# Kernel tuning notes

Hardware: AMD Instinct MI355X
Metric: run time of the kernel (lower is better)

The kernel has to match this reference:

```python
import jax, jax.numpy as jnp
import numpy as np
from jax import lax

NUM_C = 100
EMB = 256
B = 64
L = 500
NSTU = 4096
N = NUM_C + 1  # skill_embedding rows / GCN node count


def gcn_conv(x, src, dst, W, b):
    # PyG GCNConv: add self-loops, symmetric deg^-1/2 norm, scatter-add at target.
    # x: [N, Fin]; src, dst: [E] (duplicates kept, as in PyG); W: [Fout, Fin]
    n = x.shape[0]
    loop = jnp.arange(n)
    s = jnp.concatenate([src, loop])
    d = jnp.concatenate([dst, loop])
    deg = jnp.zeros((n,), x.dtype).at[d].add(1.0)
    dinv = jnp.where(deg > 0, lax.rsqrt(deg), 0.0)
    norm = dinv[s] * dinv[d]  # [E+N]
    h = x @ W.T
    out = jnp.zeros((n, h.shape[1]), x.dtype).at[d].add(norm[:, None] * h[s])
    return out + b


def rnn(x, Wih, Whh, bih, bhh):
    # torch.nn.RNN (tanh, batch_first): h_t = tanh(x_t Wih^T + bih + h_{t-1} Whh^T + bhh)
    h0 = jnp.zeros((x.shape[0], Whh.shape[0]), x.dtype)
    def step(h, xt):
        h = jnp.tanh(xt @ Wih.T + bih + h @ Whh.T + bhh)
        return h, h
    _, hs = lax.scan(step, h0, jnp.swapaxes(x, 0, 1))
    return jnp.swapaxes(hs, 0, 1)


def next_pred(res, skill):
    # (res * one_hot(next_skill)).sum(-1); row NUM_C of the one-hot table is all-zero padding
    ns = skill[:, 1:]
    p = jnp.take_along_axis(res, jnp.minimum(ns, NUM_C - 1)[..., None], axis=-1)[..., 0]
    return jnp.where(ns == NUM_C, 0.0, p)


def _forward(student, skill, answer, G, skill_emb, answer_emb, stu,
             hg_w1, hg_b1, hg_w2, hg_b2, gcn_w1, gcn_b1, gcn_w2, gcn_b2,
             w1_w, w1_b, w2_w, w2_b, fc_d_w, fc_d_b, fc_h_w, fc_h_b,
             fc_e_w, fc_e_b, pos, dg_wih, dg_whh, dg_bih, dg_bhh,
             hgr_wih, hgr_whh, hgr_bih, hgr_bhh):
    mask = (answer != 2)[..., None].astype(jnp.float32)  # [B,L,1]
    src, dst = skill[:, :-1], skill[:, 1:]               # per-sample edge lists [B,L-1]

    # HGNN over student hypergraph (eval mode: dropout = identity): x' = G (x W + b)
    h = jax.nn.relu(G @ (stu @ hg_w1.T + hg_b1))
    stu_embedding = G @ (h @ hg_w2.T + hg_b2)            # [NSTU, EMB]

    se = skill_emb[skill]                                # [B,L,EMB]
    ae = answer_emb[answer]
    skill_answer = jnp.concatenate([se, ae], -1)
    answer_skill = jnp.concatenate([ae, se], -1)
    stu_h = stu_embedding[student - 1]                   # one_hot @ table == gather, [B,L,EMB]

    # per-sample 2-layer GCN over the shared skill embedding table, vmapped over batch
    gcn2 = jax.vmap(lambda s, d: gcn_conv(
        jax.nn.relu(gcn_conv(skill_emb, s, d, gcn_w1, gcn_b1)), s, d, gcn_w2, gcn_b2))
    all_h = gcn2(src, dst)                               # [B,N,EMB]

    g = jnp.take_along_axis(all_h, skill[..., None], axis=1) * mask  # [B,L,EMB]
    lengths = mask.sum(axis=1)[:, 0].astype(jnp.int32)   # effective lengths [B]
    expand_pos = pos[lengths - 1]                        # [B,L,1] (L==500)
    expand_pos = jax.nn.softmax(expand_pos * mask, axis=1)
    pooled = (g * expand_pos).sum(axis=1)                # [B,EMB]
    pooled = jnp.broadcast_to(pooled[:, None, :], (B, L, EMB))

    x = jnp.where((answer == 1)[..., None], skill_answer, answer_skill)  # [B,L,2E]
    h_dg = rnn(jnp.concatenate([pooled, x], -1), dg_wih, dg_whh, dg_bih, dg_bhh)
    h_hg = rnn(jnp.concatenate([stu_h, x], -1), hgr_wih, hgr_whh, hgr_bih, hgr_bhh)

    logit_h = h_hg @ fc_h_w.T + fc_h_b
    logit_d = h_dg @ fc_d_w.T + fc_d_b
    theta = jax.nn.sigmoid(h_hg @ w1_w.T + w1_b + h_dg @ w2_w.T + w2_b)
    ens = jnp.concatenate([theta * h_hg, (1.0 - theta) * h_dg], -1) @ fc_e_w.T + fc_e_b
    return (next_pred(logit_h[:, :-1], skill),
            next_pred(logit_d[:, :-1], skill),
            next_pred(ens[:, :-1], skill))


def setup_inputs() -> dict:
    key = jax.random.key(0)
    ks = jax.random.split(key, 24)
    f = lambda i, shape, s=0.05: jax.random.normal(ks[i], shape, jnp.float32) * s
    return {
        "student": jax.random.randint(ks[0], (B, L), 1, NSTU + 1),
        "skill": jax.random.randint(ks[1], (B, L), 0, N),
        "answer": jax.random.randint(ks[2], (B, L), 0, 3),
        "G": f(3, (NSTU, NSTU), 0.01),
        "skill_emb": f(4, (N, EMB), 1.0),
        "answer_emb": f(5, (3, EMB), 1.0),
        "stu": f(6, (NSTU, EMB), 1.0),
        "hg_w1": f(7, (EMB, EMB)), "hg_b1": jnp.zeros((EMB,), jnp.float32),
        "hg_w2": f(8, (EMB, EMB)), "hg_b2": jnp.zeros((EMB,), jnp.float32),
        "gcn_w1": f(9, (8, EMB)), "gcn_b1": jnp.zeros((8,), jnp.float32),
        "gcn_w2": f(10, (EMB, 8)), "gcn_b2": jnp.zeros((EMB,), jnp.float32),
        "w1_w": f(11, (EMB, EMB)), "w1_b": jnp.zeros((EMB,), jnp.float32),
        "w2_w": f(12, (EMB, EMB)), "w2_b": jnp.zeros((EMB,), jnp.float32),
        "fc_d_w": f(13, (NUM_C, EMB)), "fc_d_b": jnp.zeros((NUM_C,), jnp.float32),
        "fc_h_w": f(14, (NUM_C, EMB)), "fc_h_b": jnp.zeros((NUM_C,), jnp.float32),
        "fc_e_w": f(15, (NUM_C, 2 * EMB)), "fc_e_b": jnp.zeros((NUM_C,), jnp.float32),
        "pos": jax.random.uniform(ks[16], (500, 500, 1), jnp.float32),
        "dg_wih": f(17, (EMB, 3 * EMB)), "dg_whh": f(18, (EMB, EMB)),
        "dg_bih": jnp.zeros((EMB,), jnp.float32), "dg_bhh": jnp.zeros((EMB,), jnp.float32),
        "hgr_wih": f(19, (EMB, 3 * EMB)), "hgr_whh": f(20, (EMB, EMB)),
        "hgr_bih": jnp.zeros((EMB,), jnp.float32), "hgr_bhh": jnp.zeros((EMB,), jnp.float32),
    }


def reference(student, skill, answer, G, skill_emb, answer_emb, stu,
              hg_w1, hg_b1, hg_w2, hg_b2, gcn_w1, gcn_b1, gcn_w2, gcn_b2,
              w1_w, w1_b, w2_w, w2_b, fc_d_w, fc_d_b, fc_h_w, fc_h_b,
              fc_e_w, fc_e_b, pos, dg_wih, dg_whh, dg_bih, dg_bhh,
              hgr_wih, hgr_whh, hgr_bih, hgr_bhh):
    return _forward(student, skill, answer, G, skill_emb, answer_emb, stu,
                    hg_w1, hg_b1, hg_w2, hg_b2, gcn_w1, gcn_b1, gcn_w2, gcn_b2,
                    w1_w, w1_b, w2_w, w2_b, fc_d_w, fc_d_b, fc_h_w, fc_h_b,
                    fc_e_w, fc_e_b, pos, dg_wih, dg_whh, dg_bih, dg_bhh,
                    hgr_wih, hgr_whh, hgr_bih, hgr_bhh)
```

## Files before the change

kernel.cpp:

```cpp
#include <hip/hip_runtime.h>
#include <cstdint>
#include <cstddef>

typedef unsigned short u16;
typedef __attribute__((ext_vector_type(8))) short short8;
typedef __attribute__((ext_vector_type(4))) short short4v;
typedef __attribute__((ext_vector_type(4))) float f32x4;

__device__ __forceinline__ float b2f(u16 u){ return __uint_as_float(((unsigned)u)<<16); }
__device__ __forceinline__ u16 f2b(float f){
    unsigned u = __float_as_uint(f);
    return (u16)((u + 0x7fffu + ((u>>16)&1u)) >> 16);
}
__device__ __forceinline__ int iclamp(int v, int lo, int hi){ return v<lo?lo:(v>hi?hi:v); }

__device__ __forceinline__ void barrier_lds(){
    asm volatile("s_waitcnt lgkmcnt(0)\n\ts_barrier" ::: "memory");
}

__device__ __forceinline__ float fast_exp2(float x){
#if __has_builtin(__builtin_amdgcn_exp2f)
    return __builtin_amdgcn_exp2f(x);
#else
    return __expf(x * 0.6931471805599453f);
#endif
}

__device__ __forceinline__ short8 ld8f(const float* p){
    f32x4 a = *(const f32x4*)p;
    f32x4 b = *(const f32x4*)(p+4);
    short8 r;
    #pragma unroll
    for(int j=0;j<4;j++){ r[j]=(short)f2b(a[j]); r[4+j]=(short)f2b(b[j]); }
    return r;
}
__device__ __forceinline__ short8 ld8f_s(const float* p, float s){
    f32x4 a = *(const f32x4*)p;
    f32x4 b = *(const f32x4*)(p+4);
    short8 r;
    #pragma unroll
    for(int j=0;j<4;j++){ r[j]=(short)f2b(a[j]*s); r[4+j]=(short)f2b(b[j]*s); }
    return r;
}
__device__ __forceinline__ short8 ld8b(const u16* p){ return *(const short8*)p; }

#define C_TANH 2.8853900817779268f

__global__ __launch_bounds__(256) void k_cvt(const float* __restrict__ in, u16* __restrict__ outp){
    const size_t i = ((size_t)blockIdx.x*256 + threadIdx.x)*8;
    *(short8*)&outp[i] = ld8f(in + i);
}

template<bool TRANSOUT, bool RELU, bool AF32, bool BF32>
__global__ __launch_bounds__(256) void gemm64(
    const void* __restrict__ A, const void* __restrict__ B,
    const float* __restrict__ bias, u16* __restrict__ C,
    int M, int N, int K, int ldb, int ldc)
{
    constexpr int BK=32;
    __shared__ u16 As[2][64][BK+8];
    __shared__ u16 Bs[2][64][BK+8];
    const int tid = threadIdx.x;
    const int bm = blockIdx.x*64, bn = blockIdx.y*64;
    const int wave = tid>>6, lane = tid&63, lm = lane&15, lg = lane>>4;
    const int wm = (wave>>1)*32, wn = (wave&1)*32;
    f32x4 acc[2][2];
    #pragma unroll
    for(int i=0;i<2;i++){ acc[i][0]=(f32x4){0.f,0.f,0.f,0.f}; acc[i][1]=(f32x4){0.f,0.f,0.f,0.f}; }

    const int arow = tid>>2, akc = (tid&3)*8;
    auto lda8 = [&](int k)->short8{
        return AF32 ? ld8f((const float*)A + (size_t)(bm+arow)*K + k+akc)
                    : ld8b((const u16*)A + (size_t)(bm+arow)*K + k+akc);
    };
    auto ldb8v = [&](int k)->short8{
        return BF32 ? ld8f((const float*)B + (size_t)(bn+arow)*ldb + k+akc)
                    : ld8b((const u16*)B + (size_t)(bn+arow)*ldb + k+akc);
    };
    *(short8*)&As[0][arow][akc] = lda8(0);
    *(short8*)&Bs[0][arow][akc] = ldb8v(0);
    barrier_lds();
    int p = 0;
    for(int k0=0;k0<K;k0+=BK){
        short8 a_n, b_n;
        const bool more = (k0+BK < K);
        if(more){ a_n = lda8(k0+BK); b_n = ldb8v(k0+BK); }
        short8 af[2], bfg[2];
        #pragma unroll
        for(int mt=0;mt<2;mt++) af[mt]  = *(const short8*)&As[p][wm+mt*16+lm][lg*8];
        #pragma unroll
        for(int nt=0;nt<2;nt++) bfg[nt] = *(const short8*)&Bs[p][wn+nt*16+lm][lg*8];
        #pragma unroll
        for(int nt=0;nt<2;nt++)
            #pragma unroll
            for(int mt=0;mt<2;mt++)
                acc[mt][nt] = __builtin_amdgcn_mfma_f32_16x16x32_bf16(af[mt], bfg[nt], acc[mt][nt], 0,0,0);
        if(more){
            *(short8*)&As[p^1][arow][akc] = a_n;
            *(short8*)&Bs[p^1][arow][akc] = b_n;
        }
        barrier_lds();
        p ^= 1;
    }
    #pragma unroll
    for(int nt=0;nt<2;nt++){
        const int col = bn+wn+nt*16+lm;
        const float bv = bias ? bias[col] : 0.f;
        #pragma unroll
        for(int mt=0;mt<2;mt++){
            const int row0 = bm+wm+mt*16+lg*4;
            #pragma unroll
            for(int r=0;r<4;r++){
                const int row = row0+r;
                float v = acc[mt][nt][r] + bv;
                if(RELU) v = fmaxf(v, 0.f);
                const size_t idx = TRANSOUT ? ((size_t)col*ldc + row) : ((size_t)row*ldc + col);
                C[idx] = f2b(v);
            }
        }
    }
}

__global__ __launch_bounds__(256) void k_h1pre(const float* __restrict__ skill_emb,
                                               const float* __restrict__ gcn_w1,
                                               float* __restrict__ h1pre)
{
    const int i = blockIdx.x*101 + threadIdx.x;
    if(threadIdx.x >= 101) return;
    const int idx = i; if(idx>=808) return;
    const int n=idx>>3, j=idx&7;
    const float* x = skill_emb + n*256;
    const float* w = gcn_w1 + j*256;
    float acc=0.f;
    for(int k=0;k<256;k+=4){
        f32x4 a = *(const f32x4*)&x[k];
        f32x4 b = *(const f32x4*)&w[k];
        acc += a.x*b.x + a.y*b.y + a.z*b.z + a.w*b.w;
    }
    h1pre[idx]=acc;
}

__global__ __launch_bounds__(256) void k_idx(const int* __restrict__ skill,
                                             const int* __restrict__ answer,
                                             const int* __restrict__ student,
                                             int* __restrict__ combo_t, int* __restrict__ sid_t)
{
    const int i = blockIdx.x*256 + threadIdx.x;
    if(i>=32000) return;
    const int t = i>>6, b = i&63;
    const int sk = iclamp(skill[b*500+t], 0, 100);
    const int an = iclamp(answer[b*500+t], 0, 2);
    const int sd = iclamp(student[b*500+t]-1, 0, 4095);
    combo_t[i] = sk*3+an;
    sid_t[i]   = sd;
}

__global__ __launch_bounds__(256) void k_gcn(
    const int* __restrict__ skill, const int* __restrict__ answer,
    const float* __restrict__ pos, const float* __restrict__ h1pre,
    const float* __restrict__ gcn_b1, const float* __restrict__ gcn_w2, const float* __restrict__ gcn_b2,
    float* __restrict__ pooled)
{
    const int b = blockIdx.x, tid = threadIdx.x;
    __shared__ int   sk[500];
    __shared__ float msk[500];
    __shared__ float coef[500];
    __shared__ float deg[101];
    __shared__ float agg1[101*8];
    __shared__ float agg2[101*8];
    __shared__ float red[256];
    __shared__ float vec8[8];
    __shared__ float sS[1];

    for(int i=tid;i<500;i+=256){
        sk[i]=iclamp(skill[b*500+i],0,100);
        msk[i] = (answer[b*500+i]!=2)?1.f:0.f;
    }
    for(int i=tid;i<101;i+=256) deg[i]=1.f;
    if(tid<8)  vec8[tid]=0.f;
    if(tid==8) sS[0]=0.f;
    __syncthreads();
    for(int e=tid;e<499;e+=256) atomicAdd(&deg[sk[e+1]], 1.f);
    __syncthreads();
    for(int i=tid;i<101;i+=256) deg[i] = rsqrtf(deg[i]);
    float cnt=0.f; for(int i=tid;i<500;i+=256) cnt += msk[i];
    __syncthreads();
    red[tid]=cnt; __syncthreads();
    for(int s=128;s>0;s>>=1){ if(tid<s) red[tid]+=red[tid+s]; __syncthreads(); }
    const int len = iclamp((int)(red[0]+0.5f), 1, 500);
    __syncthreads();
    for(int i=tid;i<808;i+=256){ const int n=i>>3; agg1[i] = deg[n]*deg[n]*h1pre[i]; }
    __syncthreads();
    for(int i=tid;i<499*8;i+=256){
        const int e=i>>3, j=i&7, s=sk[e], d=sk[e+1];
        atomicAdd(&agg1[d*8+j], deg[s]*deg[d]*h1pre[s*8+j]);
    }
    __syncthreads();
    for(int i=tid;i<808;i+=256){ const int j=i&7; agg1[i] = fmaxf(agg1[i]+gcn_b1[j], 0.f); }
    __syncthreads();
    for(int i=tid;i<808;i+=256){ const int n=i>>3; agg2[i] = deg[n]*deg[n]*agg1[i]; }
    __syncthreads();
    for(int i=tid;i<499*8;i+=256){
        const int e=i>>3, j=i&7, s=sk[e], d=sk[e+1];
        atomicAdd(&agg2[d*8+j], deg[s]*deg[d]*agg1[s*8+j]);
    }
    const size_t prow = (size_t)(len-1)*500;
    float vmax = -1e30f;
    for(int i=tid;i<500;i+=256){ const float v = pos[prow+i]*msk[i]; coef[i]=v; vmax=fmaxf(vmax,v); }
    red[tid]=vmax; __syncthreads();
    for(int s=128;s>0;s>>=1){ if(tid<s) red[tid]=fmaxf(red[tid],red[tid+s]); __syncthreads(); }
    const float m = red[0]; __syncthreads();
    float lsum=0.f;
    for(int i=tid;i<500;i+=256){ const float e=__expf(coef[i]-m); coef[i]=e; lsum+=e; }
    red[tid]=lsum; __syncthreads();
    for(int s=128;s>0;s>>=1){ if(tid<s) red[tid]+=red[tid+s]; __syncthreads(); }
    const float inv = 1.f/red[0];
    __syncthreads();
    float v8[8]={0,0,0,0,0,0,0,0}; float ls=0.f;
    for(int i=tid;i<500;i+=256){
        const float ci = coef[i]*inv*msk[i];
        if(ci!=0.f){
            const int n=sk[i]; ls+=ci;
            #pragma unroll
            for(int j=0;j<8;j++) v8[j] += ci*agg2[n*8+j];
        }
    }
    #pragma unroll
    for(int j=0;j<8;j++) atomicAdd(&vec8[j], v8[j]);
    atomicAdd(&sS[0], ls);
    __syncthreads();
    {
        const int o = tid;
        float acc = gcn_b2[o]*sS[0];
        #pragma unroll
        for(int j=0;j<8;j++) acc += vec8[j]*gcn_w2[o*8+j];
        pooled[b*256+o] = acc;
    }
}

__global__ __launch_bounds__(256) void k_table2(
    const float* __restrict__ skill_emb, const float* __restrict__ answer_emb,
    const float* __restrict__ wih_dg, const float* __restrict__ bih_dg, const float* __restrict__ bhh_dg,
    const float* __restrict__ wih_hg, const float* __restrict__ bih_hg, const float* __restrict__ bhh_hg,
    float* __restrict__ table_dg, float* __restrict__ table_hg)
{
    const int combo = blockIdx.x, tid = threadIdx.x, which = blockIdx.y;
    const float* wih = which ? wih_hg : wih_dg;
    const float* bih = which ? bih_hg : bih_dg;
    const float* bhh = which ? bhh_hg : bhh_dg;
    float* table     = which ? table_hg : table_dg;
    const int sid = combo/3, ans = combo - sid*3;
    __shared__ float sf[256], sg[256];
    sf[tid] = (ans==1) ? skill_emb[(size_t)sid*256+tid] : answer_emb[(size_t)ans*256+tid];
    sg[tid] = (ans==1) ? answer_emb[(size_t)ans*256+tid] : skill_emb[(size_t)sid*256+tid];
    __syncthreads();
    const int o = tid;
    float acc = bih[o] + bhh[o];
    const float* w = wih + (size_t)o*768;
    for(int k=0;k<256;k+=4){
        f32x4 w1v = *(const f32x4*)&w[256+k];
        f32x4 w2v = *(const f32x4*)&w[512+k];
        acc += sf[k]*w1v.x + sf[k+1]*w1v.y + sf[k+2]*w1v.z + sf[k+3]*w1v.w;
        acc += sg[k]*w2v.x + sg[k+1]*w2v.y + sg[k+2]*w2v.z + sg[k+3]*w2v.w;
    }
    table[(size_t)combo*256 + o] = acc;
}

__global__ __launch_bounds__(256) void k_pooledproj(const float* __restrict__ pooled,
                                                    const float* __restrict__ wih,
                                                    u16* __restrict__ outp)
{
    const int b=blockIdx.x, tid=threadIdx.x;
    __shared__ float p[256];
    p[tid] = pooled[b*256+tid];
    __syncthreads();
    const float* w = wih + (size_t)tid*768;
    float acc=0.f;
    for(int k=0;k<256;k+=4){
        f32x4 wv = *(const f32x4*)&w[k];
        acc += p[k]*wv.x + p[k+1]*wv.y + p[k+2]*wv.z + p[k+3]*wv.w;
    }
    outp[b*256+tid]=f2b(acc);
}

__global__ __launch_bounds__(256) void k_pre(
    const int* __restrict__ combo_t, const int* __restrict__ sid_t,
    const float* __restrict__ table_dg, const float* __restrict__ table_hg,
    const u16* __restrict__ pooled_proj, const u16* __restrict__ stu_proj,
    u16* __restrict__ pre_dg, u16* __restrict__ pre_hg)
{
    const int t = blockIdx.x, rnn = blockIdx.y, c = threadIdx.x;
    const int b0 = blockIdx.z*16;
    const float* tab = rnn ? table_hg : table_dg;
    u16* outp = rnn ? pre_hg : pre_dg;
    for(int b=b0;b<b0+16;b++){
        const int cmb = combo_t[t*64+b];
        const u16* prow = rnn ? (stu_proj + (size_t)sid_t[t*64+b]*256)
                              : (pooled_proj + (size_t)b*256);
        const float v = (tab[(size_t)cmb*256 + c] + b2f(prow[c])) * C_TANH;
        outp[((size_t)t*64+b)*256 + c] = f2b(v);
    }
}

__global__ __launch_bounds__(1024) void k_rnn(
    const u16* __restrict__ pre_dg, const u16* __restrict__ pre_hg,
    const float* __restrict__ whh_dg, const float* __restrict__ whh_hg,
    u16* __restrict__ hall_dg, u16* __restrict__ hall_hg)
{
    __shared__ u16 hc[2][8][4][16][8];
    const int bid = blockIdx.x;
    const int rnn = bid>>2, grp = bid&3, rb = grp*16;
    const float* W   = rnn ? whh_hg : whh_dg;
    const u16*  pre  = rnn ? pre_hg : pre_dg;
    u16*        out  = rnn ? hall_hg : hall_dg;
    const int tid = threadIdx.x, wave = tid>>6, lane = tid&63;
    const int lm = lane&15, lg = lane>>4;
    const int cb = wave*16;

    short8 wf[8];
    #pragma unroll
    for(int kk=0;kk<8;kk++)
        wf[kk] = ld8f_s(W + (size_t)(cb+lm)*256 + kk*32 + lg*8, C_TANH);

    for(int i=tid;i<2*8*4*16*8/2;i+=1024) ((unsigned*)hc)[i]=0;

    const size_t base = (size_t)(rb+lm)*256 + cb + lg*4;
    const int wchunk = wave>>1, wsub = (wave&1)*2 + (lg>>1), wslot = (lg&1)*4;

    const u16* pp = pre + base;
    u16*       op = out + base;
    uint2 pv = *(const uint2*)pp;
    pp += 16384;
    __syncthreads();

    auto stepf = [&](const u16 (&S)[8][4][16][8], u16 (&D)[8][4][16][8],
                     uint2 pvi, const u16* ppi, u16* opi)->uint2 {
        f32x4 a0, c0 = (f32x4){0.f,0.f,0.f,0.f};
        a0[0] = __uint_as_float(pvi.x << 16);
        a0[1] = __uint_as_float(pvi.x & 0xffff0000u);
        a0[2] = __uint_as_float(pvi.y << 16);
        a0[3] = __uint_as_float(pvi.y & 0xffff0000u);
        #pragma unroll
        for(int kk=0;kk<4;kk++){
            short8 hb = *(const short8*)&S[kk][lg][lm][0];
            a0 = __builtin_amdgcn_mfma_f32_16x16x32_bf16(wf[kk], hb, a0, 0,0,0);
        }
        #pragma unroll
        for(int kk=4;kk<8;kk++){
            short8 hb = *(const short8*)&S[kk][lg][lm][0];
            c0 = __builtin_amdgcn_mfma_f32_16x16x32_bf16(wf[kk], hb, c0, 0,0,0);
        }
        const uint2 pvn = *(const uint2*)ppi;
        float th[4];
        #pragma unroll
        for(int r=0;r<4;r++){
            const float x = a0[r] + c0[r];
            const float e = fast_exp2(x);
            th[r] = fmaf(-2.f, __builtin_amdgcn_rcpf(e + 1.f), 1.f);
        }
        uint2 pk;
        asm("v_cvt_pk_bf16_f32 %0, %1, %2" : "=v"(pk.x) : "v"(th[0]), "v"(th[1]));
        asm("v_cvt_pk_bf16_f32 %0, %1, %2" : "=v"(pk.y) : "v"(th[2]), "v"(th[3]));
        *(uint2*)&D[wchunk][wsub][lm][wslot] = pk;
        *(uint2*)opi = pk;
        barrier_lds();
        return pvn;
    };

    for(int t=0;t<500;t+=2){
        pv = stepf(hc[0], hc[1], pv, pp, op);  pp += 16384; op += 16384;
        pv = stepf(hc[1], hc[0], pv, pp, op);  pp += 16384; op += 16384;
    }
}

__global__ __launch_bounds__(256) void k_theta(
    const u16* __restrict__ Ah, const u16* __restrict__ Ad,
    const float* __restrict__ w1, const float* __restrict__ w2,
    const float* __restrict__ b1, const float* __restrict__ b2,
    u16* __restrict__ theta)
{
    constexpr int BK=32;
    __shared__ u16 AsH[128][BK+8];
    __shared__ u16 AsD[128][BK+8];
    __shared__ u16 BsH[64][BK+8];
    __shared__ u16 BsD[64][BK+8];
    const int tid = threadIdx.x;
    const int bm = blockIdx.x*128, bn = blockIdx.y*64;
    const int wave = tid>>6, lane = tid&63, lm = lane&15, lg = lane>>4;
    const int wm = (wave>>1)*64, wn = (wave&1)*32;
    f32x4 acc[4][2];
    #pragma unroll
    for(int i=0;i<4;i++){ acc[i][0]=(f32x4){0.f,0.f,0.f,0.f}; acc[i][1]=(f32x4){0.f,0.f,0.f,0.f}; }

    const int arow0 = tid>>2, akc0 = (tid&3)*8;
    const int arow1 = arow0 + 64;
    for(int k0=0;k0<256;k0+=BK){
        *(short8*)&AsH[arow0][akc0] = ld8b(Ah + (size_t)(bm+arow0)*256 + k0+akc0);
        *(short8*)&AsH[arow1][akc0] = ld8b(Ah + (size_t)(bm+arow1)*256 + k0+akc0);
        *(short8*)&AsD[arow0][akc0] = ld8b(Ad + (size_t)(bm+arow0)*256 + k0+akc0);
        *(short8*)&AsD[arow1][akc0] = ld8b(Ad + (size_t)(bm+arow1)*256 + k0+akc0);
        *(short8*)&BsH[arow0][akc0] = ld8f(w1 + (size_t)(bn+arow0)*256 + k0+akc0);
        *(short8*)&BsD[arow0][akc0] = ld8f(w2 + (size_t)(bn+arow0)*256 + k0+akc0);
        __syncthreads();
        short8 afH[4], afD[4], bf1[2], bf2[2];
        #pragma unroll
        for(int mt=0;mt<4;mt++){
            afH[mt] = *(const short8*)&AsH[wm+mt*16+lm][lg*8];
            afD[mt] = *(const short8*)&AsD[wm+mt*16+lm][lg*8];
        }
        #pragma unroll
        for(int nt=0;nt<2;nt++){
            bf1[nt] = *(const short8*)&BsH[wn+nt*16+lm][lg*8];
            bf2[nt] = *(const short8*)&BsD[wn+nt*16+lm][lg*8];
        }
        #pragma unroll
        for(int nt=0;nt<2;nt++)
            #pragma unroll
            for(int mt=0;mt<4;mt++){
                acc[mt][nt] = __builtin_amdgcn_mfma_f32_16x16x32_bf16(afH[mt], bf1[nt], acc[mt][nt], 0,0,0);
                acc[mt][nt] = __builtin_amdgcn_mfma_f32_16x16x32_bf16(afD[mt], bf2[nt], acc[mt][nt], 0,0,0);
            }
        __syncthreads();
    }
    #pragma unroll
    for(int nt=0;nt<2;nt++){
        const int col = bn+wn+nt*16+lm;
        const float bb = b1[col]+b2[col];
        #pragma unroll
        for(int mt=0;mt<4;mt++){
            const int row0 = bm+wm+mt*16+lg*4;
            #pragma unroll
            for(int r=0;r<4;r++){
                const float x = acc[mt][nt][r] + bb;
                theta[(size_t)(row0+r)*256 + col] = f2b(1.f/(1.f+__expf(-x)));
            }
        }
    }
}

__global__ __launch_bounds__(256) void k_out(
    const int* __restrict__ skill,
    const u16* __restrict__ hall_hg, const u16* __restrict__ hall_dg,
    const u16* __restrict__ theta,
    const float* __restrict__ fc_h_w, const float* __restrict__ fc_h_b,
    const float* __restrict__ fc_d_w, const float* __restrict__ fc_d_b,
    const float* __restrict__ fc_e_w, const float* __restrict__ fc_e_b,
    float* __restrict__ outp)
{
    const int tid=threadIdx.x, lane=tid&63;
    const int wid = blockIdx.x*4 + (tid>>6);
    const int b = wid/499, t = wid - b*499;
    const int ns = skill[b*500 + t + 1];
    float o0=0.f,o1=0.f,o2=0.f,bh=0.f,bd=0.f,be=0.f;
    if(ns != 100){
        const int c = iclamp(ns, 0, 99);
        const size_t r = (size_t)t*64 + b;
        const int k = lane*4;
        short4v hh  = *(const short4v*)&hall_hg[r*256+k];
        short4v hd  = *(const short4v*)&hall_dg[r*256+k];
        short4v th  = *(const short4v*)&theta[r*256+k];
        f32x4 fh  = *(const f32x4*)&fc_h_w[(size_t)c*256+k];
        f32x4 fd  = *(const f32x4*)&fc_d_w[(size_t)c*256+k];
        f32x4 fe1 = *(const f32x4*)&fc_e_w[(size_t)c*512+k];
        f32x4 fe2 = *(const f32x4*)&fc_e_w[(size_t)c*512+256+k];
        #pragma unroll
        for(int j=0;j<4;j++){
            const float hhj=b2f((u16)hh[j]), hdj=b2f((u16)hd[j]), tj=b2f((u16)th[j]);
            o0 += hhj*fh[j];
            o1 += hdj*fd[j];
            o2 += tj*hhj*fe1[j] + (1.f-tj)*hdj*fe2[j];
        }
        #pragma unroll
        for(int off=32;off>0;off>>=1){
            o0 += __shfl_down(o0,off);
            o1 += __shfl_down(o1,off);
            o2 += __shfl_down(o2,off);
        }
        bh=fc_h_b[c]; bd=fc_d_b[c]; be=fc_e_b[c];
    }
    if(lane==0){
        outp[            b*499+t] = (ns==100)?0.f:(o0+bh);
        outp[31936     + b*499+t] = (ns==100)?0.f:(o1+bd);
        outp[2*31936   + b*499+t] = (ns==100)?0.f:(o2+be);
    }
}

extern "C" void kernel_launch(void* const* d_in, const int* in_sizes, int n_in,
                              void* d_out, int out_size, void* d_ws, size_t ws_size,
                              hipStream_t stream)
{
    const int* student = (const int*)d_in[0];
    const int* skill   = (const int*)d_in[1];
    const int* answer  = (const int*)d_in[2];
    const float* G        = (const float*)d_in[3];
    const float* skill_emb= (const float*)d_in[4];
    const float* answer_emb=(const float*)d_in[5];
    const float* stu      = (const float*)d_in[6];
    const float* hg_w1    = (const float*)d_in[7];
    const float* hg_b1    = (const float*)d_in[8];
    const float* hg_w2    = (const float*)d_in[9];
    const float* hg_b2    = (const float*)d_in[10];
    const float* gcn_w1   = (const float*)d_in[11];
    const float* gcn_b1   = (const float*)d_in[12];
    const float* gcn_w2   = (const float*)d_in[13];
    const float* gcn_b2   = (const float*)d_in[14];
    const float* w1_w     = (const float*)d_in[15];
    const float* w1_b     = (const float*)d_in[16];
    const float* w2_w     = (const float*)d_in[17];
    const float* w2_b     = (const float*)d_in[18];
    const float* fc_d_w   = (const float*)d_in[19];
    const float* fc_d_b   = (const float*)d_in[20];
    const float* fc_h_w   = (const float*)d_in[21];
    const float* fc_h_b   = (const float*)d_in[22];
    const float* fc_e_w   = (const float*)d_in[23];
    const float* fc_e_b   = (const float*)d_in[24];
    const float* pos      = (const float*)d_in[25];
    const float* dg_wih   = (const float*)d_in[26];
    const float* dg_whh   = (const float*)d_in[27];
    const float* dg_bih   = (const float*)d_in[28];
    const float* dg_bhh   = (const float*)d_in[29];
    const float* hgr_wih  = (const float*)d_in[30];
    const float* hgr_whh  = (const float*)d_in[31];
    const float* hgr_bih  = (const float*)d_in[32];
    const float* hgr_bhh  = (const float*)d_in[33];

    char* ws = (char*)d_ws;
    size_t off = 0;
    auto nxt = [&](size_t bytes)->char*{
        char* r = ws + off;
        off += (bytes + 255) & ~(size_t)255;
        return r;
    };
    float* h1pre      = (float*)nxt(808*4);
    float* pooled     = (float*)nxt(64*256*4);
    float* table_dg   = (float*)nxt(303*256*4);
    float* table_hg   = (float*)nxt(303*256*4);
    u16*   tmpT       = (u16*)  nxt((size_t)256*4096*2);
    u16*   hbuf       = (u16*)  nxt((size_t)4096*256*2);
    u16*   stu_proj   = (u16*)  nxt((size_t)4096*256*2);
    u16*   pooled_proj= (u16*)  nxt(64*256*2);
    int*   combo_t    = (int*)  nxt(32000*4);
    int*   sid_t      = (int*)  nxt(32000*4);
    u16*   Gb         = (u16*)  nxt((size_t)4096*4096*2);
    u16*   hall_dg    = (u16*)  nxt((size_t)32000*256*2);
    u16*   hall_hg    = (u16*)  nxt((size_t)32000*256*2);
    u16*   pre_dg     = Gb;
    u16*   pre_hg     = Gb + (size_t)32000*256;
    u16*   theta      = pre_dg;

    k_h1pre<<<8,256,0,stream>>>(skill_emb, gcn_w1, h1pre);
    k_gcn<<<64,256,0,stream>>>(skill, answer, pos, h1pre, gcn_b1, gcn_w2, gcn_b2, pooled);
    k_table2<<<dim3(303,2),256,0,stream>>>(skill_emb, answer_emb,
                                           dg_wih, dg_bih, dg_bhh,
                                           hgr_wih, hgr_bih, hgr_bhh,
                                           table_dg, table_hg);
    k_idx<<<125,256,0,stream>>>(skill, answer, student, combo_t, sid_t);
    k_cvt<<<8192,256,0,stream>>>(G, Gb);

    gemm64<true ,false,true ,true ><<<dim3(64,4),256,0,stream>>>(stu,  hg_w1, hg_b1, tmpT, 4096,256,256,  256, 4096);
    gemm64<false,true ,false,false><<<dim3(64,4),256,0,stream>>>(Gb,   tmpT,  nullptr, hbuf, 4096,256,4096, 4096, 256);
    gemm64<true ,false,false,true ><<<dim3(64,4),256,0,stream>>>(hbuf, hg_w2, hg_b2, tmpT, 4096,256,256,  256, 4096);
    gemm64<false,false,false,false><<<dim3(64,4),256,0,stream>>>(Gb,   tmpT,  nullptr, hbuf, 4096,256,4096, 4096, 256);
    gemm64<false,false,false,true ><<<dim3(64,4),256,0,stream>>>(hbuf, hgr_wih, nullptr, stu_proj, 4096,256,256, 768, 256);

    k_pooledproj<<<64,256,0,stream>>>(pooled, dg_wih, pooled_proj);

    k_pre<<<dim3(500,2,4),256,0,stream>>>(combo_t, sid_t, table_dg, table_hg,
                                          pooled_proj, stu_proj, pre_dg, pre_hg);

    k_rnn<<<8,1024,0,stream>>>(pre_dg, pre_hg, dg_whh, hgr_whh, hall_dg, hall_hg);

    k_theta<<<dim3(250,4),256,0,stream>>>(hall_hg, hall_dg, w1_w, w2_w, w1_b, w2_b, theta);
    k_out<<<7984,256,0,stream>>>(skill, hall_hg, hall_dg, theta,
                                 fc_h_w, fc_h_b, fc_d_w, fc_d_b, fc_e_w, fc_e_b,
                                 (float*)d_out);
}
```

Baseline: 804.5 us.

## Fuse prep kernels, fold pooled projection into GCN, read fp32 G directly

Merges the table, index and h1pre kernels into one launch and folds the pooled-projection matvec into the GCN kernel's epilogue. It also drops the separate fp32-to-bf16 conversion of the 4096x4096 G matrix, so the two big GEMMs load fp32 G and convert it while staging tiles. This removes several launches and a 64MB read plus 32MB write conversion pass. The trade-off is that both G GEMMs now each read 64MB of fp32 instead of 32MB of bf16 and convert in the inner loop.

Measured after the change: 862.4 us. 1.07x slower.

```diff
diff --git a/kernel.cpp b/kernel.cpp
--- a/kernel.cpp
+++ b/kernel.cpp
@@ -45,11 +45,6 @@
 __device__ __forceinline__ short8 ld8b(const u16* p){ return *(const short8*)p; }
 
 #define C_TANH 2.8853900817779268f
-
-__global__ __launch_bounds__(256) void k_cvt(const float* __restrict__ in, u16* __restrict__ outp){
-    const size_t i = ((size_t)blockIdx.x*256 + threadIdx.x)*8;
-    *(short8*)&outp[i] = ld8f(in + i);
-}
 
 template<bool TRANSOUT, bool RELU, bool AF32, bool BF32>
 __global__ __launch_bounds__(256) void gemm64(
@@ -121,45 +116,70 @@
     }
 }
 
-__global__ __launch_bounds__(256) void k_h1pre(const float* __restrict__ skill_emb,
-                                               const float* __restrict__ gcn_w1,
-                                               float* __restrict__ h1pre)
-{
-    const int i = blockIdx.x*101 + threadIdx.x;
-    if(threadIdx.x >= 101) return;
-    const int idx = i; if(idx>=808) return;
-    const int n=idx>>3, j=idx&7;
-    const float* x = skill_emb + n*256;
-    const float* w = gcn_w1 + j*256;
-    float acc=0.f;
-    for(int k=0;k<256;k+=4){
-        f32x4 a = *(const f32x4*)&x[k];
-        f32x4 b = *(const f32x4*)&w[k];
-        acc += a.x*b.x + a.y*b.y + a.z*b.z + a.w*b.w;
-    }
-    h1pre[idx]=acc;
-}
-
-__global__ __launch_bounds__(256) void k_idx(const int* __restrict__ skill,
-                                             const int* __restrict__ answer,
-                                             const int* __restrict__ student,
-                                             int* __restrict__ combo_t, int* __restrict__ sid_t)
-{
-    const int i = blockIdx.x*256 + threadIdx.x;
-    if(i>=32000) return;
-    const int t = i>>6, b = i&63;
-    const int sk = iclamp(skill[b*500+t], 0, 100);
-    const int an = iclamp(answer[b*500+t], 0, 2);
-    const int sd = iclamp(student[b*500+t]-1, 0, 4095);
-    combo_t[i] = sk*3+an;
-    sid_t[i]   = sd;
+__global__ __launch_bounds__(256) void k_prep(
+    const float* __restrict__ skill_emb, const float* __restrict__ answer_emb,
+    const float* __restrict__ wih_dg, const float* __restrict__ bih_dg, const float* __restrict__ bhh_dg,
+    const float* __restrict__ wih_hg, const float* __restrict__ bih_hg, const float* __restrict__ bhh_hg,
+    const float* __restrict__ gcn_w1,
+    const int* __restrict__ skill, const int* __restrict__ answer, const int* __restrict__ student,
+    float* __restrict__ table_dg, float* __restrict__ table_hg,
+    float* __restrict__ h1pre, int* __restrict__ combo_t, int* __restrict__ sid_t)
+{
+    const int bid = blockIdx.x, tid = threadIdx.x;
+    if(bid < 606){
+        const int which = (bid >= 303) ? 1 : 0;
+        const int combo = bid - which*303;
+        const float* wih = which ? wih_hg : wih_dg;
+        const float* bih = which ? bih_hg : bih_dg;
+        const float* bhh = which ? bhh_hg : bhh_dg;
+        float* table     = which ? table_hg : table_dg;
+        const int sid = combo/3, ans = combo - sid*3;
+        __shared__ float sf[256], sg[256];
+        sf[tid] = (ans==1) ? skill_emb[(size_t)sid*256+tid] : answer_emb[(size_t)ans*256+tid];
+        sg[tid] = (ans==1) ? answer_emb[(size_t)ans*256+tid] : skill_emb[(size_t)sid*256+tid];
+        __syncthreads();
+        const int o = tid;
+        float acc = bih[o] + bhh[o];
+        const float* w = wih + (size_t)o*768;
+        for(int k=0;k<256;k+=4){
+            f32x4 w1v = *(const f32x4*)&w[256+k];
+            f32x4 w2v = *(const f32x4*)&w[512+k];
+            acc += sf[k]*w1v.x + sf[k+1]*w1v.y + sf[k+2]*w1v.z + sf[k+3]*w1v.w;
+            acc += sg[k]*w2v.x + sg[k+1]*w2v.y + sg[k+2]*w2v.z + sg[k+3]*w2v.w;
+        }
+        table[(size_t)combo*256 + o] = acc;
+    } else if(bid < 731){
+        const int i = (bid-606)*256 + tid;
+        if(i>=32000) return;
+        const int t = i>>6, b = i&63;
+        const int sk = iclamp(skill[b*500+t], 0, 100);
+        const int an = iclamp(answer[b*500+t], 0, 2);
+        const int sd = iclamp(student[b*500+t]-1, 0, 4095);
+        combo_t[i] = sk*3+an;
+        sid_t[i]   = sd;
+    } else {
+        if(tid >= 101) return;
+        const int idx = (bid-731)*101 + tid;
+        if(idx>=808) return;
+        const int n=idx>>3, j=idx&7;
+        const float* x = skill_emb + n*256;
+        const float* w = gcn_w1 + j*256;
+        float acc=0.f;
+        for(int k=0;k<256;k+=4){
+            f32x4 a = *(const f32x4*)&x[k];
+            f32x4 b = *(const f32x4*)&w[k];
+            acc += a.x*b.x + a.y*b.y + a.z*b.z + a.w*b.w;
+        }
+        h1pre[idx]=acc;
+    }
 }
 
 __global__ __launch_bounds__(256) void k_gcn(
     const int* __restrict__ skill, const int* __restrict__ answer,
     const float* __restrict__ pos, const float* __restrict__ h1pre,
     const float* __restrict__ gcn_b1, const float* __restrict__ gcn_w2, const float* __restrict__ gcn_b2,
-    float* __restrict__ pooled)
+    const float* __restrict__ wih_dg,
+    u16* __restrict__ pooled_proj)
 {
     const int b = blockIdx.x, tid = threadIdx.x;
     __shared__ int   sk[500];
@@ -234,53 +254,19 @@
         float acc = gcn_b2[o]*sS[0];
         #pragma unroll
         for(int j=0;j<8;j++) acc += vec8[j]*gcn_w2[o*8+j];
-        pooled[b*256+o] = acc;
-    }
-}
-
-__global__ __launch_bounds__(256) void k_table2(
-    const float* __restrict__ skill_emb, const float* __restrict__ answer_emb,
-    const float* __restrict__ wih_dg, const float* __restrict__ bih_dg, const float* __restrict__ bhh_dg,
-    const float* __restrict__ wih_hg, const float* __restrict__ bih_hg, const float* __restrict__ bhh_hg,
-    float* __restrict__ table_dg, float* __restrict__ table_hg)
-{
-    const int combo = blockIdx.x, tid = threadIdx.x, which = blockIdx.y;
-    const float* wih = which ? wih_hg : wih_dg;
-    const float* bih = which ? bih_hg : bih_dg;
-    const float* bhh = which ? bhh_hg : bhh_dg;
-    float* table     = which ? table_hg : table_dg;
-    const int sid = combo/3, ans = combo - sid*3;
-    __shared__ float sf[256], sg[256];
-    sf[tid] = (ans==1) ? skill_emb[(size_t)sid*256+tid] : answer_emb[(size_t)ans*256+tid];
-    sg[tid] = (ans==1) ? answer_emb[(size_t)ans*256+tid] : skill_emb[(size_t)sid*256+tid];
-    __syncthreads();
-    const int o = tid;
-    float acc = bih[o] + bhh[o];
-    const float* w = wih + (size_t)o*768;
-    for(int k=0;k<256;k+=4){
-        f32x4 w1v = *(const f32x4*)&w[256+k];
-        f32x4 w2v = *(const f32x4*)&w[512+k];
-        acc += sf[k]*w1v.x + sf[k+1]*w1v.y + sf[k+2]*w1v.z + sf[k+3]*w1v.w;
-        acc += sg[k]*w2v.x + sg[k+1]*w2v.y + sg[k+2]*w2v.z + sg[k+3]*w2v.w;
-    }
-    table[(size_t)combo*256 + o] = acc;
-}
-
-__global__ __launch_bounds__(256) void k_pooledproj(const float* __restrict__ pooled,
-                                                    const float* __restrict__ wih,
-                                                    u16* __restrict__ outp)
-{
-    const int b=blockIdx.x, tid=threadIdx.x;
-    __shared__ float p[256];
-    p[tid] = pooled[b*256+tid];
-    __syncthreads();
-    const float* w = wih + (size_t)tid*768;
-    float acc=0.f;
-    for(int k=0;k<256;k+=4){
-        f32x4 wv = *(const f32x4*)&w[k];
-        acc += p[k]*wv.x + p[k+1]*wv.y + p[k+2]*wv.z + p[k+3]*wv.w;
-    }
-    outp[b*256+tid]=f2b(acc);
+        red[o] = acc;
+    }
+    __syncthreads();
+    {
+        const int o = tid;
+        const float* w = wih_dg + (size_t)o*768;
+        float acc=0.f;
+        for(int k=0;k<256;k+=4){
+            f32x4 wv = *(const f32x4*)&w[k];
+            acc += red[k]*wv.x + red[k+1]*wv.y + red[k+2]*wv.z + red[k+3]*wv.w;
+        }
+        pooled_proj[b*256+o]=f2b(acc);
+    }
 }
 
 __global__ __launch_bounds__(256) void k_pre(
@@ -532,7 +518,6 @@
         return r;
     };
     float* h1pre      = (float*)nxt(808*4);
-    float* pooled     = (float*)nxt(64*256*4);
     float* table_dg   = (float*)nxt(303*256*4);
     float* table_hg   = (float*)nxt(303*256*4);
     u16*   tmpT       = (u16*)  nxt((size_t)256*4096*2);
@@ -541,29 +526,25 @@
     u16*   pooled_proj= (u16*)  nxt(64*256*2);
     int*   combo_t    = (int*)  nxt(32000*4);
     int*   sid_t      = (int*)  nxt(32000*4);
-    u16*   Gb         = (u16*)  nxt((size_t)4096*4096*2);
+    u16*   pre_dg     = (u16*)  nxt((size_t)32000*256*2);
+    u16*   pre_hg     = (u16*)  nxt((size_t)32000*256*2);
     u16*   hall_dg    = (u16*)  nxt((size_t)32000*256*2);
     u16*   hall_hg    = (u16*)  nxt((size_t)32000*256*2);
-    u16*   pre_dg     = Gb;
-    u16*   pre_hg     = Gb + (size_t)32000*256;
     u16*   theta      = pre_dg;
 
-    k_h1pre<<<8,256,0,stream>>>(skill_emb, gcn_w1, h1pre);
-    k_gcn<<<64,256,0,stream>>>(skill, answer, pos, h1pre, gcn_b1, gcn_w2, gcn_b2, pooled);
-    k_table2<<<dim3(303,2),256,0,stream>>>(skill_emb, answer_emb,
-                                           dg_wih, dg_bih, dg_bhh,
-                                           hgr_wih, hgr_bih, hgr_bhh,
-                                           table_dg, table_hg);
-    k_idx<<<125,256,0,stream>>>(skill, answer, student, combo_t, sid_t);
-    k_cvt<<<8192,256,0,stream>>>(G, Gb);
+    k_prep<<<739,256,0,stream>>>(skill_emb, answer_emb,
+                                 dg_wih, dg_bih, dg_bhh,
+                                 hgr_wih, hgr_bih, hgr_bhh,
+                                 gcn_w1, skill, answer, student,
+                                 table_dg, table_hg, h1pre, combo_t, sid_t);
+    k_gcn<<<64,256,0,stream>>>(skill, answer, pos, h1pre, gcn_b1, gcn_w2, gcn_b2,
+                               dg_wih, pooled_proj);
 
     gemm64<true ,false,true ,true ><<<dim3(64,4),256,0,stream>>>(stu,  hg_w1, hg_b1, tmpT, 4096,256,256,  256, 4096);
-    gemm64<false,true ,false,false><<<dim3(64,4),256,0,stream>>>(Gb,   tmpT,  nullptr, hbuf, 4096,256,4096, 4096, 256);
+    gemm64<false,true ,true ,false><<<dim3(64,4),256,0,stream>>>(G,    tmpT,  nullptr, hbuf, 4096,256,4096, 4096, 256);
     gemm64<true ,false,false,true ><<<dim3(64,4),256,0,stream>>>(hbuf, hg_w2, hg_b2, tmpT, 4096,256,256,  256, 4096);
-    gemm64<false,false,false,false><<<dim3(64,4),256,0,stream>>>(Gb,   tmpT,  nullptr, hbuf, 4096,256,4096, 4096, 256);
+    gemm64<false,false,true ,false><<<dim3(64,4),256,0,stream>>>(G,    tmpT,  nullptr, hbuf, 4096,256,4096, 4096, 256);
     gemm64<false,false,false,true ><<<dim3(64,4),256,0,stream>>>(hbuf, hgr_wih, nullptr, stu_proj, 4096,256,256, 768, 256);
-
-    k_pooledproj<<<64,256,0,stream>>>(pooled, dg_wih, pooled_proj);
 
     k_pre<<<dim3(500,2,4),256,0,stream>>>(combo_t, sid_t, table_dg, table_hg,
                                           pooled_proj, stu_proj, pre_dg, pre_hg);
```
